# Performance work log

Measured on AMD Instinct MI355X. Metric: run time of the kernel, lower is better.

Reference implementation:

```python
import jax, jax.numpy as jnp
import numpy as np

D_MODEL = 768
BOTTLENECK = 64
LN_EPS = 1e-5
SCALE = 1.0


def setup_inputs() -> dict:
    key = jax.random.key(0)
    k_x, k_wd = jax.random.split(key, 2)
    x = jax.random.normal(k_x, (8, 4096, D_MODEL), dtype=jnp.float32)
    # LayerNorm affine params
    ln_gamma = jnp.ones((D_MODEL,), dtype=jnp.float32)
    ln_beta = jnp.zeros((D_MODEL,), dtype=jnp.float32)
    # down_proj: kaiming_uniform_(a=sqrt(5)) -> bound = 1/sqrt(fan_in)
    bound = 1.0 / np.sqrt(D_MODEL)
    w_down = jax.random.uniform(k_wd, (D_MODEL, BOTTLENECK), dtype=jnp.float32,
                                minval=-bound, maxval=bound)
    b_down = jnp.zeros((BOTTLENECK,), dtype=jnp.float32)
    # up_proj initialized to zeros per 'lora' init; use small nonzero to make grads informative?
    # Stay faithful: zeros, as in the module's init.
    w_up = jnp.zeros((BOTTLENECK, D_MODEL), dtype=jnp.float32)
    b_up = jnp.zeros((D_MODEL,), dtype=jnp.float32)
    return {"x": x, "ln_gamma": ln_gamma, "ln_beta": ln_beta,
            "w_down": w_down, "b_down": b_down, "w_up": w_up, "b_up": b_up}


def _layer_norm(x, gamma, beta):
    mean = jnp.mean(x, axis=-1, keepdims=True)
    var = jnp.var(x, axis=-1, keepdims=True)
    return (x - mean) * jax.lax.rsqrt(var + LN_EPS) * gamma + beta


def reference(x, ln_gamma, ln_beta, w_down, b_down, w_up, b_up):
    # adapter_layernorm_option == 'in': LN before down projection
    h = _layer_norm(x, ln_gamma, ln_beta)              # [B, S, D]
    down = jnp.einsum('bsd,dk->bsk', h, w_down) + b_down  # [B, S, K]
    down = jax.nn.relu(down)
    # dropout is identity in eval mode
    out = jnp.einsum('bsk,kd->bsd', down, w_up) + b_up    # [B, S, D]
    return out * SCALE
```

## Files before the change

kernel.cpp:

```cpp
#include <hip/hip_runtime.h>
#include <hip/hip_bf16.h>


#define D_MODEL 768
#define KB      64
#define NTHR    256
#define PPAD    72

#define CH1     4
#define NCH1    6
#define CH2     6
#define NCH2    8

typedef __attribute__((ext_vector_type(8))) short    bf16x8;
typedef __attribute__((ext_vector_type(4))) float    f32x4;
typedef __attribute__((ext_vector_type(4))) unsigned short us4;

static __device__ __forceinline__ unsigned short f2bf(float f) {
  unsigned int u = __builtin_bit_cast(unsigned int, f);
  unsigned int r = u + 0x7FFFu + ((u >> 16) & 1u);
  return (unsigned short)(r >> 16);
}

__global__ void __launch_bounds__(1024) adapter_prep(
    const float* __restrict__ wd,
    const float* __restrict__ wu,
    const float* __restrict__ gamma,
    const float* __restrict__ beta,
    const float* __restrict__ bdown,
    unsigned short* __restrict__ wdT,
    unsigned short* __restrict__ wuT,
    float* __restrict__ s_arr,
    float* __restrict__ t_arr) {
  const int b = blockIdx.x;
  const int t = threadIdx.x;
  if (b < 48) {
    const int i = b * 1024 + t;
    const int k1 = i / D_MODEL;
    const int d1 = i - k1 * D_MODEL;
    wdT[i] = f2bf(gamma[d1] * wd[(size_t)d1 * KB + k1]);
    const int d2 = i >> 6;
    const int k2 = i & 63;
    wuT[i] = f2bf(wu[(size_t)k2 * D_MODEL + d2]);
  } else {
    const int k = t & 63;
    const int c = t >> 6;
    float ss = 0.f, tt = 0.f;
    const int d0 = c * 48;
    #pragma unroll 4
    for (int d = d0; d < d0 + 48; ++d) {
      const float w = wd[(size_t)d * KB + k];
      ss = fmaf(gamma[d], w, ss);
      tt = fmaf(beta[d],  w, tt);
    }
    __shared__ float ps[16][64], pt[16][64];
    ps[c][k] = ss; pt[c][k] = tt;
    __syncthreads();
    if (t < 64) {
      float S = 0.f, T = 0.f;
      #pragma unroll
      for (int q = 0; q < 16; ++q) { S += ps[q][t]; T += pt[q][t]; }
      s_arr[t] = S;
      t_arr[t] = T + bdown[t];
    }
  }
}

__global__ void __launch_bounds__(NTHR, 2) adapter_main(
    const float* __restrict__ x,
    const float* __restrict__ s_arr,
    const float* __restrict__ t_arr,
    const unsigned short* __restrict__ wdT,
    const unsigned short* __restrict__ wuT,
    const float* __restrict__ b_up,
    float* __restrict__ out) {

  __shared__ unsigned short p_s[4][16][PPAD];

  const int t   = threadIdx.x;
  const int wid = t >> 6;
  const int l   = t & 63;
  const int lr  = l & 15;
  const int lg  = l >> 4;
  const int row0 = blockIdx.x * 64 + wid * 16;

  const float* xp = x + (size_t)(row0 + lr) * D_MODEL + 8 * lg;
  const unsigned short* wp = wdT + (size_t)lr * D_MODEL + 8 * lg;

  f32x4 acc[4];
  #pragma unroll
  for (int c = 0; c < 4; ++c) acc[c] = (f32x4){0.f, 0.f, 0.f, 0.f};
  float s1 = 0.f, s2 = 0.f;

  float4 xb[2][CH1][2];
  bf16x8 wf[2][4];

  #pragma unroll
  for (int j = 0; j < CH1; ++j) {
    xb[0][j][0] = *(const float4*)(xp + 32 * j);
    xb[0][j][1] = *(const float4*)(xp + 32 * j + 4);
  }
  #pragma unroll
  for (int c = 0; c < 4; ++c) {
    wf[0][c] = *(const bf16x8*)(wp + (size_t)16 * c * D_MODEL);
    wf[1][c] = *(const bf16x8*)(wp + (size_t)16 * c * D_MODEL + 32);
  }

  #pragma unroll
  for (int ch = 0; ch < NCH1; ++ch) {
    const int cur = ch & 1, nxt = cur ^ 1;
    if (ch < NCH1 - 1) {
      #pragma unroll
      for (int j = 0; j < CH1; ++j) {
        xb[nxt][j][0] = *(const float4*)(xp + 32 * (CH1 * (ch + 1) + j));
        xb[nxt][j][1] = *(const float4*)(xp + 32 * (CH1 * (ch + 1) + j) + 4);
      }
    }
    #pragma unroll
    for (int j = 0; j < CH1; ++j) {
      const int kk = CH1 * ch + j;
      const float4 v0 = xb[cur][j][0];
      const float4 v1 = xb[cur][j][1];
      s1 += (v0.x + v0.y) + (v0.z + v0.w) + (v1.x + v1.y) + (v1.z + v1.w);
      s2 = fmaf(v0.x, v0.x, s2); s2 = fmaf(v0.y, v0.y, s2);
      s2 = fmaf(v0.z, v0.z, s2); s2 = fmaf(v0.w, v0.w, s2);
      s2 = fmaf(v1.x, v1.x, s2); s2 = fmaf(v1.y, v1.y, s2);
      s2 = fmaf(v1.z, v1.z, s2); s2 = fmaf(v1.w, v1.w, s2);
      bf16x8 xf;
      xf[0] = (short)f2bf(v0.x); xf[1] = (short)f2bf(v0.y);
      xf[2] = (short)f2bf(v0.z); xf[3] = (short)f2bf(v0.w);
      xf[4] = (short)f2bf(v1.x); xf[5] = (short)f2bf(v1.y);
      xf[6] = (short)f2bf(v1.z); xf[7] = (short)f2bf(v1.w);
      #pragma unroll
      for (int c = 0; c < 4; ++c)
        acc[c] = __builtin_amdgcn_mfma_f32_16x16x32_bf16(wf[kk & 1][c], xf, acc[c], 0, 0, 0);
      if (kk + 2 < 24) {
        #pragma unroll
        for (int c = 0; c < 4; ++c)
          wf[kk & 1][c] = *(const bf16x8*)(wp + (size_t)16 * c * D_MODEL + 32 * (kk + 2));
      }
    }
  }

  s1 += __shfl_xor(s1, 16); s1 += __shfl_xor(s1, 32);
  s2 += __shfl_xor(s2, 16); s2 += __shfl_xor(s2, 32);
  const float mu  = s1 * (1.0f / 768.0f);
  const float var = s2 * (1.0f / 768.0f) - mu * mu;
  const float rs  = rsqrtf(var + 1e-5f);
  const float nm  = -rs * mu;

  #pragma unroll
  for (int c = 0; c < 4; ++c) {
    const float4 sv = *(const float4*)(s_arr + 16 * c + 4 * lg);
    const float4 tv = *(const float4*)(t_arr + 16 * c + 4 * lg);
    us4 pk;
    pk.x = f2bf(fmaxf(fmaf(rs, acc[c][0], fmaf(nm, sv.x, tv.x)), 0.f));
    pk.y = f2bf(fmaxf(fmaf(rs, acc[c][1], fmaf(nm, sv.y, tv.y)), 0.f));
    pk.z = f2bf(fmaxf(fmaf(rs, acc[c][2], fmaf(nm, sv.z, tv.z)), 0.f));
    pk.w = f2bf(fmaxf(fmaf(rs, acc[c][3], fmaf(nm, sv.w, tv.w)), 0.f));
    *(us4*)&p_s[wid][lr][16 * c + 4 * lg] = pk;
  }

  const bf16x8 pa0 = *(const bf16x8*)&p_s[wid][lr][8 * lg];
  const bf16x8 pa1 = *(const bf16x8*)&p_s[wid][lr][32 + 8 * lg];
  float* op = out + (size_t)(row0 + 4 * lg) * D_MODEL + lr;

  bf16x8 wb[2][CH2][2];
  float  bb[2][CH2];
  #pragma unroll
  for (int j = 0; j < CH2; ++j) {
    const int cn = 16 * j;
    const unsigned short* bp = wuT + (size_t)(cn + lr) * KB + 8 * lg;
    wb[0][j][0] = *(const bf16x8*)(bp);
    wb[0][j][1] = *(const bf16x8*)(bp + 32);
    bb[0][j]    = b_up[cn + lr];
  }

  #pragma unroll
  for (int ch = 0; ch < NCH2; ++ch) {
    const int cur = ch & 1, nxt = cur ^ 1;
    if (ch < NCH2 - 1) {
      #pragma unroll
      for (int j = 0; j < CH2; ++j) {
        const int cn = 16 * (CH2 * (ch + 1) + j);
        const unsigned short* bp = wuT + (size_t)(cn + lr) * KB + 8 * lg;
        wb[nxt][j][0] = *(const bf16x8*)(bp);
        wb[nxt][j][1] = *(const bf16x8*)(bp + 32);
        bb[nxt][j]    = b_up[cn + lr];
      }
    }
    #pragma unroll
    for (int j = 0; j < CH2; ++j) {
      const int cn = 16 * (CH2 * ch + j);
      f32x4 c0 = {0.f, 0.f, 0.f, 0.f};
      c0 = __builtin_amdgcn_mfma_f32_16x16x32_bf16(pa0, wb[cur][j][0], c0, 0, 0, 0);
      c0 = __builtin_amdgcn_mfma_f32_16x16x32_bf16(pa1, wb[cur][j][1], c0, 0, 0, 0);
      const float bu = bb[cur][j];
      op[(size_t)0 * D_MODEL + cn] = c0[0] + bu;
      op[(size_t)1 * D_MODEL + cn] = c0[1] + bu;
      op[(size_t)2 * D_MODEL + cn] = c0[2] + bu;
      op[(size_t)3 * D_MODEL + cn] = c0[3] + bu;
    }
  }
}

extern "C" void kernel_launch(void* const* d_in, const int* in_sizes, int n_in,
                              void* d_out, int out_size, void* d_ws, size_t ws_size,
                              hipStream_t stream) {
  const float* x     = (const float*)d_in[0];
  const float* gamma = (const float*)d_in[1];
  const float* beta  = (const float*)d_in[2];
  const float* wd    = (const float*)d_in[3];
  const float* bdown = (const float*)d_in[4];
  const float* wu    = (const float*)d_in[5];
  const float* bup   = (const float*)d_in[6];
  float* out = (float*)d_out;

  char* ws = (char*)d_ws;
  unsigned short* wdT = (unsigned short*)ws;
  unsigned short* wuT = (unsigned short*)(ws + 98304);
  float* s_arr = (float*)(ws + 196608);
  float* t_arr = (float*)(ws + 196864);

  const int rows = in_sizes[0] / D_MODEL;

  adapter_prep<<<49, 1024, 0, stream>>>(wd, wu, gamma, beta, bdown,
                                        wdT, wuT, s_arr, t_arr);
  adapter_main<<<rows / 64, NTHR, 0, stream>>>(x, s_arr, t_arr, wdT, wuT, bup, out);
}
```

Measured before the change: 221.9 us.

## Stream x tiles into LDS via global_load_lds double buffering

Replaces register-staged global loads of x in the first GEMM with direct global-to-LDS async loads (global_load_lds, 16 bytes) into a per-wave double buffer, then reads fragments back from LDS. Weight fragments for each chunk are now loaded into registers up front per chunk instead of being rolling-prefetched. The aim is to cut VGPR pressure and issue overhead for the streaming input, at the cost of 64KB of LDS per block, a full vmcnt(0) wait each chunk, and extra LDS reads. The large LDS footprint may limit occupancy, and the vmcnt(0) wait serialises the prefetch with compute.

```diff
diff --git a/kernel.cpp b/kernel.cpp
--- a/kernel.cpp
+++ b/kernel.cpp
@@ -7,8 +7,6 @@
 #define NTHR    256
 #define PPAD    72
 
-#define CH1     4
-#define NCH1    6
 #define CH2     6
 #define NCH2    8
 
@@ -20,6 +18,12 @@
   unsigned int u = __builtin_bit_cast(unsigned int, f);
   unsigned int r = u + 0x7FFFu + ((u >> 16) & 1u);
   return (unsigned short)(r >> 16);
+}
+
+static __device__ __forceinline__ void gload16(const void* g, void* l) {
+  __builtin_amdgcn_global_load_lds(
+      (const __attribute__((address_space(1))) unsigned int*)g,
+      (__attribute__((address_space(3))) unsigned int*)l, 16, 0, 0);
 }
 
 __global__ void __launch_bounds__(1024) adapter_prep(
@@ -75,6 +79,7 @@
     const float* __restrict__ b_up,
     float* __restrict__ out) {
 
+  __shared__ __align__(16) unsigned char xs[4][2][8192];
   __shared__ unsigned short p_s[4][16][PPAD];
 
   const int t   = threadIdx.x;
@@ -84,7 +89,9 @@
   const int lg  = l >> 4;
   const int row0 = blockIdx.x * 64 + wid * 16;
 
-  const float* xp = x + (size_t)(row0 + lr) * D_MODEL + 8 * lg;
+  const float* xlane = x + (size_t)(row0 + lr) * D_MODEL + lg * 4;
+  unsigned char* xb[2] = { &xs[wid][0][0], &xs[wid][1][0] };
+
   const unsigned short* wp = wdT + (size_t)lr * D_MODEL + 8 * lg;
 
   f32x4 acc[4];
@@ -92,53 +99,45 @@
   for (int c = 0; c < 4; ++c) acc[c] = (f32x4){0.f, 0.f, 0.f, 0.f};
   float s1 = 0.f, s2 = 0.f;
 
-  float4 xb[2][CH1][2];
-  bf16x8 wf[2][4];
-
-  #pragma unroll
-  for (int j = 0; j < CH1; ++j) {
-    xb[0][j][0] = *(const float4*)(xp + 32 * j);
-    xb[0][j][1] = *(const float4*)(xp + 32 * j + 4);
-  }
-  #pragma unroll
-  for (int c = 0; c < 4; ++c) {
-    wf[0][c] = *(const bf16x8*)(wp + (size_t)16 * c * D_MODEL);
-    wf[1][c] = *(const bf16x8*)(wp + (size_t)16 * c * D_MODEL + 32);
-  }
-
-  #pragma unroll
-  for (int ch = 0; ch < NCH1; ++ch) {
-    const int cur = ch & 1, nxt = cur ^ 1;
-    if (ch < NCH1 - 1) {
-      #pragma unroll
-      for (int j = 0; j < CH1; ++j) {
-        xb[nxt][j][0] = *(const float4*)(xp + 32 * (CH1 * (ch + 1) + j));
-        xb[nxt][j][1] = *(const float4*)(xp + 32 * (CH1 * (ch + 1) + j) + 4);
-      }
-    }
+  #pragma unroll
+  for (int n = 0; n < 8; ++n)
+    gload16(xlane + 32 * (n >> 1) + 16 * (n & 1), xb[0] + 1024 * n);
+
+  #pragma unroll
+  for (int ch = 0; ch < 6; ++ch) {
+    const int cur = ch & 1;
+    bf16x8 wf[4][4];
     #pragma unroll
-    for (int j = 0; j < CH1; ++j) {
-      const int kk = CH1 * ch + j;
-      const float4 v0 = xb[cur][j][0];
-      const float4 v1 = xb[cur][j][1];
-      s1 += (v0.x + v0.y) + (v0.z + v0.w) + (v1.x + v1.y) + (v1.z + v1.w);
-      s2 = fmaf(v0.x, v0.x, s2); s2 = fmaf(v0.y, v0.y, s2);
-      s2 = fmaf(v0.z, v0.z, s2); s2 = fmaf(v0.w, v0.w, s2);
-      s2 = fmaf(v1.x, v1.x, s2); s2 = fmaf(v1.y, v1.y, s2);
-      s2 = fmaf(v1.z, v1.z, s2); s2 = fmaf(v1.w, v1.w, s2);
+    for (int c = 0; c < 4; ++c)
+      #pragma unroll
+      for (int j = 0; j < 4; ++j)
+        wf[j][c] = *(const bf16x8*)(wp + (size_t)16 * c * D_MODEL + 32 * (4 * ch + j));
+    if (ch < 5) {
+      const float* g = xlane + 128 * (ch + 1);
+      #pragma unroll
+      for (int n = 0; n < 8; ++n)
+        gload16(g + 32 * (n >> 1) + 16 * (n & 1), xb[cur ^ 1] + 1024 * n);
+    }
+    asm volatile("s_waitcnt vmcnt(0)" ::: "memory");
+    __builtin_amdgcn_sched_barrier(0);
+    #pragma unroll
+    for (int j = 0; j < 4; ++j) {
+      const unsigned char* cb = xb[cur] + 2048 * j + 512 * lg + 16 * lr;
+      const f32x4 va = *(const f32x4*)(cb);
+      const f32x4 vb = *(const f32x4*)(cb + 256);
+      s1 += (va[0] + va[1]) + (va[2] + va[3]) + (vb[0] + vb[1]) + (vb[2] + vb[3]);
+      s2 = fmaf(va[0], va[0], s2); s2 = fmaf(va[1], va[1], s2);
+      s2 = fmaf(va[2], va[2], s2); s2 = fmaf(va[3], va[3], s2);
+      s2 = fmaf(vb[0], vb[0], s2); s2 = fmaf(vb[1], vb[1], s2);
+      s2 = fmaf(vb[2], vb[2], s2); s2 = fmaf(vb[3], vb[3], s2);
       bf16x8 xf;
-      xf[0] = (short)f2bf(v0.x); xf[1] = (short)f2bf(v0.y);
-      xf[2] = (short)f2bf(v0.z); xf[3] = (short)f2bf(v0.w);
-      xf[4] = (short)f2bf(v1.x); xf[5] = (short)f2bf(v1.y);
-      xf[6] = (short)f2bf(v1.z); xf[7] = (short)f2bf(v1.w);
+      xf[0] = (short)f2bf(va[0]); xf[1] = (short)f2bf(va[1]);
+      xf[2] = (short)f2bf(va[2]); xf[3] = (short)f2bf(va[3]);
+      xf[4] = (short)f2bf(vb[0]); xf[5] = (short)f2bf(vb[1]);
+      xf[6] = (short)f2bf(vb[2]); xf[7] = (short)f2bf(vb[3]);
       #pragma unroll
       for (int c = 0; c < 4; ++c)
-        acc[c] = __builtin_amdgcn_mfma_f32_16x16x32_bf16(wf[kk & 1][c], xf, acc[c], 0, 0, 0);
-      if (kk + 2 < 24) {
-        #pragma unroll
-        for (int c = 0; c < 4; ++c)
-          wf[kk & 1][c] = *(const bf16x8*)(wp + (size_t)16 * c * D_MODEL + 32 * (kk + 2));
-      }
+        acc[c] = __builtin_amdgcn_mfma_f32_16x16x32_bf16(wf[j][c], xf, acc[c], 0, 0, 0);
     }
   }
 
@@ -175,7 +174,6 @@
     wb[0][j][1] = *(const bf16x8*)(bp + 32);
     bb[0][j]    = b_up[cn + lr];
   }
-
   #pragma unroll
   for (int ch = 0; ch < NCH2; ++ch) {
     const int cur = ch & 1, nxt = cur ^ 1;
```

Result: no change. 224.4 us (+1.1%).
